# Kernel optimization log

Hardware: AMD Instinct MI355X
Metric: run time of the kernel (lower is better)

The kernel has to match this reference:

```python
import jax, jax.numpy as jnp
import numpy as np

N_HEAD = 16
N_EMBD = 1024
B, T = 4, 1024


def setup_inputs() -> dict:
    key = jax.random.key(0)
    ks = jax.random.split(key, 8)
    hs = N_EMBD // N_HEAD
    x = jax.random.normal(ks[0], (B, T, N_EMBD), dtype=jnp.float32)
    # previous-layer attention load per token, ~O(1/T) like a softmax column mean
    refractory_state = jax.random.uniform(ks[1], (B, T), dtype=jnp.float32) / T
    s_attn = 1.0 / np.sqrt(N_EMBD)
    W_attn = jax.random.normal(ks[2], (N_EMBD, 3 * N_EMBD), dtype=jnp.float32) * s_attn
    b_attn = jnp.zeros((3 * N_EMBD,), dtype=jnp.float32)
    W_proj = jax.random.normal(ks[3], (N_EMBD, N_EMBD), dtype=jnp.float32) * s_attn
    b_proj = jnp.zeros((N_EMBD,), dtype=jnp.float32)
    # learnable LIF params, init per module (lif_mode='refractory')
    threshold = jnp.full((N_HEAD,), 0.01, dtype=jnp.float32)
    leak = jnp.full((N_HEAD,), 2.0, dtype=jnp.float32)
    steepness = jnp.full((N_HEAD,), 2.0, dtype=jnp.float32)
    ref_strength = jnp.full((N_HEAD,), -2.0, dtype=jnp.float32)
    cross_w = jnp.full((N_HEAD,), -2.0, dtype=jnp.float32)
    return {
        "x": x, "refractory_state": refractory_state,
        "W_attn": W_attn, "b_attn": b_attn,
        "W_proj": W_proj, "b_proj": b_proj,
        "threshold": threshold, "leak": leak, "steepness": steepness,
        "ref_strength": ref_strength, "cross_w": cross_w,
    }


def reference(x, refractory_state, W_attn, b_attn, W_proj, b_proj,
              threshold, leak, steepness, ref_strength, cross_w):
    Bq, Tq, C = x.shape
    H = N_HEAD
    hs = C // H
    qkv = x @ W_attn + b_attn                     # [B,T,3C]
    q, k, v = jnp.split(qkv, 3, axis=-1)
    q = q.reshape(Bq, Tq, H, hs).transpose(0, 2, 1, 3)  # [B,H,T,hs]
    k = k.reshape(Bq, Tq, H, hs).transpose(0, 2, 1, 3)
    v = v.reshape(Bq, Tq, H, hs).transpose(0, 2, 1, 3)

    att = jnp.einsum('bhqd,bhkd->bhqk', q, k) * (1.0 / jnp.sqrt(jnp.asarray(hs, x.dtype)))
    causal = jnp.tril(jnp.ones((Tq, Tq), dtype=bool))
    att = jnp.where(causal[None, None], att, -jnp.inf)
    probs = jax.nn.softmax(att, axis=-1)          # [B,H,T,T]

    thr = (jnp.abs(threshold) * 0.1)[None, :, None, None]
    lk = jax.nn.sigmoid(leak)[None, :, None, None]
    st = jax.nn.softplus(steepness)[None, :, None, None]
    # refractory: column load over queries + cross-layer load
    column_load = probs.mean(axis=-2, keepdims=True)          # [B,H,1,T]
    eff_thr = thr + jax.nn.softplus(ref_strength)[None, :, None, None] * column_load
    eff_thr = eff_thr + jax.nn.sigmoid(cross_w)[None, :, None, None] * refractory_state[:, None, None, :]

    fire = jax.nn.sigmoid(st * (probs - eff_thr))
    lif_w = fire + lk * (1.0 - fire)
    mod = probs * lif_w
    mod = mod / (mod.sum(axis=-1, keepdims=True) + 1e-8)
    new_refractory = mod.mean(axis=1).mean(axis=-2)           # [B,T]

    y = jnp.einsum('bhqk,bhkd->bhqd', mod, v)
    y = y.transpose(0, 2, 1, 3).reshape(Bq, Tq, C)
    y = y @ W_proj + b_proj
    return y, new_refractory
```

## Files before the change

kernel.cpp:

```cpp
#include <hip/hip_runtime.h>
#include <math.h>

#define B_  4
#define T_  1024
#define C_  1024
#define H_  16
#define HS_ 64
#define K2E 0.1803368801f
#define LOG2E 1.44269504f

typedef _Float16 f16;
typedef _Float16 f16x8 __attribute__((ext_vector_type(8)));
typedef float f32x4 __attribute__((ext_vector_type(4)));

#define MFMA16(a,b,c) __builtin_amdgcn_mfma_f32_16x16x32_f16(a,b,c,0,0,0)
#define EXP2(x) __builtin_amdgcn_exp2f(x)
#define RCP(x)  __builtin_amdgcn_rcpf(x)

__device__ __forceinline__ void gload16(const f16* g, f16* l){
    __builtin_amdgcn_global_load_lds(
        (const __attribute__((address_space(1))) void*)g,
        (__attribute__((address_space(3))) void*)l, 16, 0, 0);
}

__device__ __forceinline__ float qsum_(float v){
    v += __shfl_xor(v,1,64); v += __shfl_xor(v,2,64);
    v += __shfl_xor(v,4,64); v += __shfl_xor(v,8,64);
    return v;
}
__device__ __forceinline__ float sigmoidf_(float x){ return 1.0f/(1.0f + __expf(-x)); }
__device__ __forceinline__ float softplusf_(float x){ return fmaxf(x, 0.0f) + log1pf(__expf(-fabsf(x))); }

__global__ __launch_bounds__(256) void conv_f16_k(
    const float* __restrict__ in, f16* __restrict__ out, int n8)
{
    int i = blockIdx.x*256 + threadIdx.x;
    if (i < n8){
        const float4* p = (const float4*)in + (size_t)i*2;
        float4 a = p[0], b = p[1];
        f16x8 o;
        o[0]=(f16)a.x; o[1]=(f16)a.y; o[2]=(f16)a.z; o[3]=(f16)a.w;
        o[4]=(f16)b.x; o[5]=(f16)b.y; o[6]=(f16)b.z; o[7]=(f16)b.w;
        *((f16x8*)out + i) = o;
    }
}

__global__ __launch_bounds__(256) void transpose_f16_k(
    const float* __restrict__ in, f16* __restrict__ out, int K, int N)
{
    __shared__ float tl[32][33];
    const int n0 = blockIdx.x*32, k0 = blockIdx.y*32;
    const int c = threadIdx.x & 31, r4 = threadIdx.x >> 5;
    #pragma unroll
    for (int i=0;i<4;i++){
        int r = r4*4 + i;
        tl[r][c] = in[(size_t)(k0+r)*N + n0 + c];
    }
    __syncthreads();
    #pragma unroll
    for (int i=0;i<4;i++){
        int r = r4*4 + i;
        out[(size_t)(n0+r)*K + k0 + c] = (f16)tl[c][r];
    }
}

__global__ __launch_bounds__(256) void gemm_qkv_k(
    const f16* __restrict__ A, const f16* __restrict__ Bt,
    const float* __restrict__ bias,
    f16* __restrict__ Qh, f16* __restrict__ Kh, f16* __restrict__ Vt)
{
    __shared__ __align__(16) f16 Al[8*512];
    __shared__ __align__(16) f16 Bl[8*512];
    const int tid = threadIdx.x;
    const int lane = tid & 63, wave = tid >> 6;
    const int lx = lane & 15, quad = lane >> 4;
    const int wm = wave & 1, wn = wave >> 1;
    const int m0 = blockIdx.y*128, n0 = blockIdx.x*128;
    f32x4 acc[4][4];
    #pragma unroll
    for (int i=0;i<4;i++){
        #pragma unroll
        for (int j=0;j<4;j++){ acc[i][j][0]=0.f;acc[i][j][1]=0.f;acc[i][j][2]=0.f;acc[i][j][3]=0.f; }
    }
    for (int k0=0; k0<1024; k0+=32){
        __syncthreads();
        #pragma unroll
        for (int i=0;i<2;i++){
            int c = i*4 + wave;
            gload16(A  + (size_t)(m0 + c*16 + lx)*1024 + k0 + quad*8, &Al[c*512]);
            gload16(Bt + (size_t)(n0 + c*16 + lx)*1024 + k0 + quad*8, &Bl[c*512]);
        }
        __syncthreads();
        f16x8 af[4], bf[4];
        #pragma unroll
        for (int mt=0;mt<4;mt++) af[mt] = *(const f16x8*)&Al[(wm*4+mt)*512 + quad*128 + lx*8];
        #pragma unroll
        for (int nt=0;nt<4;nt++) bf[nt] = *(const f16x8*)&Bl[(wn*4+nt)*512 + quad*128 + lx*8];
        #pragma unroll
        for (int mt=0;mt<4;mt++){
            #pragma unroll
            for (int nt=0;nt<4;nt++)
                acc[mt][nt] = MFMA16(af[mt], bf[nt], acc[mt][nt]);
        }
    }
    #pragma unroll
    for (int mt=0;mt<4;mt++){
        #pragma unroll
        for (int nt=0;nt<4;nt++){
            int n = n0 + wn*64 + nt*16 + lx;
            int which = n >> 10, cc = n & 1023, h = cc >> 6, d = cc & 63;
            float bv = bias[n];
            #pragma unroll
            for (int r=0;r<4;r++){
                int m = m0 + wm*64 + mt*16 + quad*4 + r;
                int bb = m >> 10, t = m & 1023;
                int bh = bb*16 + h;
                float v = acc[mt][nt][r] + bv;
                if (which==0)      Qh[((size_t)bh*1024 + t)*64 + d] = (f16)v;
                else if (which==1) Kh[((size_t)bh*1024 + t)*64 + d] = (f16)v;
                else               Vt[((size_t)bh*64 + d)*1024 + t] = (f16)v;
            }
        }
    }
}

__global__ __launch_bounds__(256) void gemm_proj_k(
    const f16* __restrict__ A, const f16* __restrict__ Bt,
    const float* __restrict__ bias, float* __restrict__ out)
{
    __shared__ __align__(16) f16 Al[8*512];
    __shared__ __align__(16) f16 Bl[4*512];
    const int tid = threadIdx.x;
    const int lane = tid & 63, wave = tid >> 6;
    const int lx = lane & 15, quad = lane >> 4;
    const int wm = wave & 1, wn = wave >> 1;
    const int m0 = blockIdx.y*128, n0 = blockIdx.x*64;
    f32x4 acc[4][2];
    #pragma unroll
    for (int i=0;i<4;i++){
        #pragma unroll
        for (int j=0;j<2;j++){ acc[i][j][0]=0.f;acc[i][j][1]=0.f;acc[i][j][2]=0.f;acc[i][j][3]=0.f; }
    }
    for (int k0=0; k0<1024; k0+=32){
        __syncthreads();
        #pragma unroll
        for (int i=0;i<3;i++){
            int u = i*4 + wave;
            if (u < 8)
                gload16(A  + (size_t)(m0 + u*16 + lx)*1024 + k0 + quad*8, &Al[u*512]);
            else
                gload16(Bt + (size_t)(n0 + (u-8)*16 + lx)*1024 + k0 + quad*8, &Bl[(u-8)*512]);
        }
        __syncthreads();
        f16x8 af[4], bf[2];
        #pragma unroll
        for (int mt=0;mt<4;mt++) af[mt] = *(const f16x8*)&Al[(wm*4+mt)*512 + quad*128 + lx*8];
        #pragma unroll
        for (int nt=0;nt<2;nt++) bf[nt] = *(const f16x8*)&Bl[(wn*2+nt)*512 + quad*128 + lx*8];
        #pragma unroll
        for (int mt=0;mt<4;mt++){
            #pragma unroll
            for (int nt=0;nt<2;nt++)
                acc[mt][nt] = MFMA16(af[mt], bf[nt], acc[mt][nt]);
        }
    }
    #pragma unroll
    for (int mt=0;mt<4;mt++){
        #pragma unroll
        for (int nt=0;nt<2;nt++){
            int n = n0 + wn*32 + nt*16 + lx;
            float bv = bias[n];
            #pragma unroll
            for (int r=0;r<4;r++){
                int m = m0 + wm*64 + mt*16 + quad*4 + r;
                out[(size_t)m*1024 + n] = acc[mt][nt][r] + bv;
            }
        }
    }
}

__global__ __launch_bounds__(256) void attn_stats_k(
    const f16* __restrict__ Qh, const f16* __restrict__ Kh,
    float* __restrict__ rowl, float* __restrict__ colp)
{
    __shared__ __align__(16) f16 Kl[4096];
    __shared__ float colacc[64];
    const int tid = threadIdx.x;
    const int lane = tid & 63, wave = tid >> 6;
    const int lx = lane & 15, quad = lane >> 4;
    const int g  = 15 - (blockIdx.x >> 6);
    const int bh = blockIdx.x & 63;
    const int qpos = wave*16 + quad*4;

    const size_t qoff = ((size_t)bh*1024 + g*64 + wave*16 + lx)*64;
    f16x8 aq0 = *(const f16x8*)(Qh + qoff + quad*8);
    f16x8 aq1 = *(const f16x8*)(Qh + qoff + 32 + quad*8);

    float ls[4] = {0.f,0.f,0.f,0.f};
    for (int kt=0; kt<=g; kt++){
        __syncthreads();
        #pragma unroll
        for (int i=0;i<2;i++){
            int u = i*4 + wave, c = u & 3, kh = u >> 2;
            gload16(Kh + ((size_t)bh*1024 + kt*64 + c*16 + lx)*64 + kh*32 + quad*8,
                    &Kl[c*1024 + kh*512]);
        }
        __syncthreads();
        const bool diag = (kt == g);
        #pragma unroll
        for (int nt=0;nt<4;nt++){
            f32x4 sc = {0.f,0.f,0.f,0.f};
            f16x8 b0 = *(const f16x8*)&Kl[nt*1024 + quad*128 + lx*8];
            f16x8 b1 = *(const f16x8*)&Kl[nt*1024 + (4+quad)*128 + lx*8];
            sc = MFMA16(aq0, b0, sc);
            sc = MFMA16(aq1, b1, sc);
            #pragma unroll
            for (int r=0;r<4;r++){
                float sv = sc[r];
                if (diag && (nt*16+lx) > (qpos + r)) sv = -1e4f;
                ls[r] += EXP2(sv*K2E);
            }
        }
    }
    float invl[4];
    #pragma unroll
    for (int r=0;r<4;r++){
        float l = qsum_(ls[r]);
        if (lx == 0) rowl[(size_t)bh*1024 + g*64 + qpos + r] = l;
        invl[r] = RCP(l);
    }

    for (int kt=0; kt<=g; kt++){
        __syncthreads();
        #pragma unroll
        for (int i=0;i<2;i++){
            int u = i*4 + wave, c = u & 3, kh = u >> 2;
            gload16(Kh + ((size_t)bh*1024 + kt*64 + c*16 + lx)*64 + kh*32 + quad*8,
                    &Kl[c*1024 + kh*512]);
        }
        if (tid < 64) colacc[tid] = 0.f;
        __syncthreads();
        const bool diag = (kt == g);
        #pragma unroll
        for (int nt=0;nt<4;nt++){
            f32x4 sc = {0.f,0.f,0.f,0.f};
            f16x8 b0 = *(const f16x8*)&Kl[nt*1024 + quad*128 + lx*8];
            f16x8 b1 = *(const f16x8*)&Kl[nt*1024 + (4+quad)*128 + lx*8];
            sc = MFMA16(aq0, b0, sc);
            sc = MFMA16(aq1, b1, sc);
            float csum = 0.f;
            #pragma unroll
            for (int r=0;r<4;r++){
                float sv = sc[r];
                if (diag && (nt*16+lx) > (qpos + r)) sv = -1e4f;
                csum += EXP2(sv*K2E) * invl[r];
            }
            csum += __shfl_xor(csum,16,64); csum += __shfl_xor(csum,32,64);
            if (quad == 0) atomicAdd(&colacc[nt*16+lx], csum);
        }
        __syncthreads();
        if (tid < 64) atomicAdd(&colp[(size_t)bh*1024 + kt*64 + tid], colacc[tid]);
    }
}

__global__ __launch_bounds__(256) void attn_apply_k(
    const f16* __restrict__ Qh, const f16* __restrict__ Kh, const f16* __restrict__ Vt,
    const float* __restrict__ rowl,
    const float* __restrict__ colp, const float* __restrict__ refr,
    const float* __restrict__ threshold, const float* __restrict__ leak,
    const float* __restrict__ steepness, const float* __restrict__ ref_strength,
    const float* __restrict__ cross_w,
    f16* __restrict__ Yh, float* __restrict__ racc)
{
    __shared__ __align__(16) f16 Kl[4096];
    __shared__ __align__(16) f16 Vl[4096];
    __shared__ __align__(16) f16 Pl[4][16*72];
    __shared__ float eb[1024];
    __shared__ float colacc[64];
    const int tid = threadIdx.x;
    const int lane = tid & 63, wave = tid >> 6;
    const int lx = lane & 15, quad = lane >> 4;
    const int g  = 15 - (blockIdx.x >> 6);
    const int bh = blockIdx.x & 63;
    const int b  = bh >> 4, h = bh & 15;
    const int qpos = wave*16 + quad*4;

    const float thr = fabsf(threshold[h])*0.1f;
    const float lk  = sigmoidf_(leak[h]);
    const float st2 = softplusf_(steepness[h]) * LOG2E;
    const float sprT= softplusf_(ref_strength[h]) * (1.0f/T_);
    const float cw  = sigmoidf_(cross_w[h]);
    const float Alk = 1.f - lk;

    {
        float4 cp = *(const float4*)(colp + (size_t)bh*1024 + tid*4);
        float4 rf = *(const float4*)(refr + (size_t)b*1024 + tid*4);
        eb[tid*4+0] = thr + sprT*cp.x + cw*rf.x;
        eb[tid*4+1] = thr + sprT*cp.y + cw*rf.y;
        eb[tid*4+2] = thr + sprT*cp.z + cw*rf.z;
        eb[tid*4+3] = thr + sprT*cp.w + cw*rf.w;
    }

    const size_t qoff = ((size_t)bh*1024 + g*64 + wave*16 + lx)*64;
    f16x8 aq0 = *(const f16x8*)(Qh + qoff + quad*8);
    f16x8 aq1 = *(const f16x8*)(Qh + qoff + 32 + quad*8);

    float invl[4];
    #pragma unroll
    for (int r=0;r<4;r++)
        invl[r] = RCP(rowl[(size_t)bh*1024 + g*64 + qpos + r]);

    f32x4 y[4];
    #pragma unroll
    for (int i=0;i<4;i++){ y[i][0]=0.f;y[i][1]=0.f;y[i][2]=0.f;y[i][3]=0.f; }
    float Dp[4] = {0.f,0.f,0.f,0.f};

    for (int kt=0; kt<=g; kt++){
        __syncthreads();
        #pragma unroll
        for (int i=0;i<4;i++){
            int u = i*4 + wave;
            if (u < 8){
                int c = u & 3, kh = u >> 2;
                gload16(Kh + ((size_t)bh*1024 + kt*64 + c*16 + lx)*64 + kh*32 + quad*8,
                        &Kl[c*1024 + kh*512]);
            } else {
                int v = u - 8, c = v & 3, kh = v >> 2;
                gload16(Vt + ((size_t)bh*64 + c*16 + lx)*1024 + kt*64 + kh*32 + quad*8,
                        &Vl[c*1024 + kh*512]);
            }
        }
        __syncthreads();
        const bool diag = (kt == g);
        #pragma unroll
        for (int nt=0;nt<4;nt++){
            f32x4 sc = {0.f,0.f,0.f,0.f};
            f16x8 b0 = *(const f16x8*)&Kl[nt*1024 + quad*128 + lx*8];
            f16x8 b1 = *(const f16x8*)&Kl[nt*1024 + (4+quad)*128 + lx*8];
            sc = MFMA16(aq0, b0, sc);
            sc = MFMA16(aq1, b1, sc);
            float ec = st2 * eb[kt*64 + nt*16 + lx];
            #pragma unroll
            for (int r=0;r<4;r++){
                float sv = sc[r];
                if (diag && (nt*16+lx) > (qpos + r)) sv = -1e4f;
                float p = EXP2(sv*K2E) * invl[r];
                float e2 = EXP2(ec - st2*p);
                float fire = RCP(1.f + e2);
                float pw = p * (lk + Alk*fire);
                Dp[r] += pw;
                Pl[wave][(quad*4+r)*72 + nt*16 + lx] = (f16)pw;
            }
        }
        f16x8 ap0 = *(const f16x8*)&Pl[wave][lx*72 + quad*8];
        f16x8 ap1 = *(const f16x8*)&Pl[wave][lx*72 + 32 + quad*8];
        #pragma unroll
        for (int dt=0;dt<4;dt++){
            f16x8 bv0 = *(const f16x8*)&Vl[dt*1024 + quad*128 + lx*8];
            f16x8 bv1 = *(const f16x8*)&Vl[dt*1024 + (4+quad)*128 + lx*8];
            y[dt] = MFMA16(ap0, bv0, y[dt]);
            y[dt] = MFMA16(ap1, bv1, y[dt]);
        }
    }
    float invD[4];
    #pragma unroll
    for (int r=0;r<4;r++) invD[r] = RCP(qsum_(Dp[r]) + 1e-8f);
    #pragma unroll
    for (int dt=0;dt<4;dt++){
        #pragma unroll
        for (int r=0;r<4;r++){
            Yh[(size_t)(b*1024 + g*64 + wave*16 + quad*4 + r)*1024 + h*64 + dt*16 + lx]
                = (f16)(y[dt][r]*invD[r]);
        }
    }

    for (int kt=0; kt<=g; kt++){
        __syncthreads();
        #pragma unroll
        for (int i=0;i<2;i++){
            int u = i*4 + wave, c = u & 3, kh = u >> 2;
            gload16(Kh + ((size_t)bh*1024 + kt*64 + c*16 + lx)*64 + kh*32 + quad*8,
                    &Kl[c*1024 + kh*512]);
        }
        if (tid < 64) colacc[tid] = 0.f;
        __syncthreads();
        const bool diag = (kt == g);
        #pragma unroll
        for (int nt=0;nt<4;nt++){
            f32x4 sc = {0.f,0.f,0.f,0.f};
            f16x8 b0 = *(const f16x8*)&Kl[nt*1024 + quad*128 + lx*8];
            f16x8 b1 = *(const f16x8*)&Kl[nt*1024 + (4+quad)*128 + lx*8];
            sc = MFMA16(aq0, b0, sc);
            sc = MFMA16(aq1, b1, sc);
            float ec = st2 * eb[kt*64 + nt*16 + lx];
            float csum = 0.f;
            #pragma unroll
            for (int r=0;r<4;r++){
                float sv = sc[r];
                if (diag && (nt*16+lx) > (qpos + r)) sv = -1e4f;
                float p = EXP2(sv*K2E) * invl[r];
                float e2 = EXP2(ec - st2*p);
                float fire = RCP(1.f + e2);
                csum += p * (lk + Alk*fire) * invD[r];
            }
            csum += __shfl_xor(csum,16,64); csum += __shfl_xor(csum,32,64);
            if (quad == 0) atomicAdd(&colacc[nt*16+lx], csum);
        }
        __syncthreads();
        if (tid < 64) atomicAdd(&racc[(size_t)b*1024 + kt*64 + tid], colacc[tid]);
    }
}

__global__ __launch_bounds__(256) void finish_refr_k(
    const float* __restrict__ racc, float* __restrict__ out)
{
    int i = blockIdx.x*256 + threadIdx.x;
    if (i < B_*T_) out[i] = racc[i] * (1.0f/(H_*T_));
}

extern "C" void kernel_launch(void* const* d_in, const int* in_sizes, int n_in,
                              void* d_out, int out_size, void* d_ws, size_t ws_size,
                              hipStream_t stream) {
    (void)in_sizes; (void)n_in; (void)out_size; (void)ws_size;
    const float* x           = (const float*)d_in[0];
    const float* refr        = (const float*)d_in[1];
    const float* W_attn      = (const float*)d_in[2];
    const float* b_attn      = (const float*)d_in[3];
    const float* W_proj      = (const float*)d_in[4];
    const float* b_proj      = (const float*)d_in[5];
    const float* threshold   = (const float*)d_in[6];
    const float* leak        = (const float*)d_in[7];
    const float* steepness   = (const float*)d_in[8];
    const float* ref_strength= (const float*)d_in[9];
    const float* cross_w     = (const float*)d_in[10];
    float* out = (float*)d_out;

    char* ws = (char*)d_ws;
    f16* x_h = (f16*)ws;                       ws += (size_t)4096*1024*2;
    f16* WaT = (f16*)ws;                       ws += (size_t)3072*1024*2;
    f16* WpT = (f16*)ws;                       ws += (size_t)1024*1024*2;
    f16* Qh  = (f16*)ws;                       ws += (size_t)64*1024*64*2;
    f16* Kh  = (f16*)ws;                       ws += (size_t)64*1024*64*2;
    f16* Vt  = (f16*)ws;                       ws += (size_t)64*64*1024*2;
    f16* Yh  = (f16*)ws;                       ws += (size_t)4096*1024*2;
    float* rowl = (float*)ws;                  ws += (size_t)65536*4;
    float* colp = (float*)ws;                  ws += (size_t)65536*4;
    float* racc = (float*)ws;                  ws += (size_t)4096*4;

    hipMemsetAsync(colp, 0, 65536*sizeof(float), stream);
    hipMemsetAsync(racc, 0, 4096*sizeof(float), stream);

    conv_f16_k<<<dim3(2048), dim3(256), 0, stream>>>(x, x_h, 4096*1024/8);
    transpose_f16_k<<<dim3(96,32), dim3(256), 0, stream>>>(W_attn, WaT, 1024, 3072);
    transpose_f16_k<<<dim3(32,32), dim3(256), 0, stream>>>(W_proj, WpT, 1024, 1024);
    gemm_qkv_k<<<dim3(24,32), dim3(256), 0, stream>>>(x_h, WaT, b_attn, Qh, Kh, Vt);
    attn_stats_k<<<dim3(1024), dim3(256), 0, stream>>>(Qh, Kh, rowl, colp);
    attn_apply_k<<<dim3(1024), dim3(256), 0, stream>>>(
        Qh, Kh, Vt, rowl, colp, refr,
        threshold, leak, steepness, ref_strength, cross_w, Yh, racc);
    gemm_proj_k<<<dim3(16,32), dim3(256), 0, stream>>>(Yh, WpT, b_proj, out);
    finish_refr_k<<<dim3(16), dim3(256), 0, stream>>>(racc, out + (size_t)B_*T_*C_);
}
```

Baseline: 319.1 us.

## Register-prefetch GEMM tiles, drop LDS staging in attention, precompute effective thresholds

The QKV and projection GEMMs now load the next K-tile into registers while the current tile is computed, replacing direct global-to-LDS loads. The QKV GEMM also uses a wider K step and a grouped block-index swizzle for L2 reuse. The attention kernels read K and V fragments straight from global memory instead of staging them through shared memory, which removes the per-tile barriers. Column sums now go into a per-block 1024-entry LDS accumulator that is flushed once at the end. A new small kernel precomputes the scaled effective threshold per (b,h,k), so the apply kernel no longer rebuilds it, at the cost of an extra launch and more global or cache traffic for the K, V and threshold reads.

```diff
diff --git a/kernel.cpp b/kernel.cpp
--- a/kernel.cpp
+++ b/kernel.cpp
@@ -16,12 +16,6 @@
 #define MFMA16(a,b,c) __builtin_amdgcn_mfma_f32_16x16x32_f16(a,b,c,0,0,0)
 #define EXP2(x) __builtin_amdgcn_exp2f(x)
 #define RCP(x)  __builtin_amdgcn_rcpf(x)
-
-__device__ __forceinline__ void gload16(const f16* g, f16* l){
-    __builtin_amdgcn_global_load_lds(
-        (const __attribute__((address_space(1))) void*)g,
-        (__attribute__((address_space(3))) void*)l, 16, 0, 0);
-}
 
 __device__ __forceinline__ float qsum_(float v){
     v += __shfl_xor(v,1,64); v += __shfl_xor(v,2,64);
@@ -69,38 +63,59 @@
     const float* __restrict__ bias,
     f16* __restrict__ Qh, f16* __restrict__ Kh, f16* __restrict__ Vt)
 {
-    __shared__ __align__(16) f16 Al[8*512];
-    __shared__ __align__(16) f16 Bl[8*512];
+    __shared__ __align__(16) f16 Al[8192];
+    __shared__ __align__(16) f16 Bl[8192];
     const int tid = threadIdx.x;
     const int lane = tid & 63, wave = tid >> 6;
     const int lx = lane & 15, quad = lane >> 4;
     const int wm = wave & 1, wn = wave >> 1;
-    const int m0 = blockIdx.y*128, n0 = blockIdx.x*128;
+    const int bid = blockIdx.x;
+    const int grp = bid >> 5, w = bid & 31;
+    const int m0 = ((grp/6)*8 + (w>>2))*128;
+    const int n0 = ((grp%6)*4 + (w&3))*128;
     f32x4 acc[4][4];
     #pragma unroll
     for (int i=0;i<4;i++){
         #pragma unroll
         for (int j=0;j<4;j++){ acc[i][j][0]=0.f;acc[i][j][1]=0.f;acc[i][j][2]=0.f;acc[i][j][3]=0.f; }
     }
-    for (int k0=0; k0<1024; k0+=32){
+    f16x8 ra[4], rb[4];
+    #pragma unroll
+    for (int i=0;i<4;i++){
+        int u = i*4 + wave, rg = u>>1, kh = u&1;
+        ra[i] = *(const f16x8*)(A  + (size_t)(m0+rg*16+lx)*1024 + kh*32 + quad*8);
+        rb[i] = *(const f16x8*)(Bt + (size_t)(n0+rg*16+lx)*1024 + kh*32 + quad*8);
+    }
+    for (int k0=0; k0<1024; k0+=64){
         __syncthreads();
         #pragma unroll
-        for (int i=0;i<2;i++){
-            int c = i*4 + wave;
-            gload16(A  + (size_t)(m0 + c*16 + lx)*1024 + k0 + quad*8, &Al[c*512]);
-            gload16(Bt + (size_t)(n0 + c*16 + lx)*1024 + k0 + quad*8, &Bl[c*512]);
+        for (int i=0;i<4;i++){
+            int u = i*4 + wave, rg = u>>1, kh = u&1;
+            *(f16x8*)&Al[rg*1024 + kh*512 + quad*128 + lx*8] = ra[i];
+            *(f16x8*)&Bl[rg*1024 + kh*512 + quad*128 + lx*8] = rb[i];
         }
         __syncthreads();
-        f16x8 af[4], bf[4];
-        #pragma unroll
-        for (int mt=0;mt<4;mt++) af[mt] = *(const f16x8*)&Al[(wm*4+mt)*512 + quad*128 + lx*8];
-        #pragma unroll
-        for (int nt=0;nt<4;nt++) bf[nt] = *(const f16x8*)&Bl[(wn*4+nt)*512 + quad*128 + lx*8];
-        #pragma unroll
-        for (int mt=0;mt<4;mt++){
-            #pragma unroll
-            for (int nt=0;nt<4;nt++)
-                acc[mt][nt] = MFMA16(af[mt], bf[nt], acc[mt][nt]);
+        if (k0 + 64 < 1024){
+            #pragma unroll
+            for (int i=0;i<4;i++){
+                int u = i*4 + wave, rg = u>>1, kh = u&1;
+                ra[i] = *(const f16x8*)(A  + (size_t)(m0+rg*16+lx)*1024 + k0+64 + kh*32 + quad*8);
+                rb[i] = *(const f16x8*)(Bt + (size_t)(n0+rg*16+lx)*1024 + k0+64 + kh*32 + quad*8);
+            }
+        }
+        #pragma unroll
+        for (int ks=0;ks<2;ks++){
+            f16x8 af[4], bf[4];
+            #pragma unroll
+            for (int mt=0;mt<4;mt++) af[mt] = *(const f16x8*)&Al[(wm*4+mt)*1024 + ks*512 + quad*128 + lx*8];
+            #pragma unroll
+            for (int nt=0;nt<4;nt++) bf[nt] = *(const f16x8*)&Bl[(wn*4+nt)*1024 + ks*512 + quad*128 + lx*8];
+            #pragma unroll
+            for (int mt=0;mt<4;mt++){
+                #pragma unroll
+                for (int nt=0;nt<4;nt++)
+                    acc[mt][nt] = MFMA16(af[mt], bf[nt], acc[mt][nt]);
+            }
         }
     }
     #pragma unroll
@@ -141,17 +156,24 @@
         #pragma unroll
         for (int j=0;j<2;j++){ acc[i][j][0]=0.f;acc[i][j][1]=0.f;acc[i][j][2]=0.f;acc[i][j][3]=0.f; }
     }
+    f16x8 ra[2], rb;
+    #pragma unroll
+    for (int i=0;i<2;i++)
+        ra[i] = *(const f16x8*)(A + (size_t)(m0 + (i*4+wave)*16 + lx)*1024 + quad*8);
+    rb = *(const f16x8*)(Bt + (size_t)(n0 + wave*16 + lx)*1024 + quad*8);
     for (int k0=0; k0<1024; k0+=32){
         __syncthreads();
         #pragma unroll
-        for (int i=0;i<3;i++){
-            int u = i*4 + wave;
-            if (u < 8)
-                gload16(A  + (size_t)(m0 + u*16 + lx)*1024 + k0 + quad*8, &Al[u*512]);
-            else
-                gload16(Bt + (size_t)(n0 + (u-8)*16 + lx)*1024 + k0 + quad*8, &Bl[(u-8)*512]);
-        }
+        for (int i=0;i<2;i++)
+            *(f16x8*)&Al[(i*4+wave)*512 + quad*128 + lx*8] = ra[i];
+        *(f16x8*)&Bl[wave*512 + quad*128 + lx*8] = rb;
         __syncthreads();
+        if (k0 + 32 < 1024){
+            #pragma unroll
+            for (int i=0;i<2;i++)
+                ra[i] = *(const f16x8*)(A + (size_t)(m0 + (i*4+wave)*16 + lx)*1024 + k0+32 + quad*8);
+            rb = *(const f16x8*)(Bt + (size_t)(n0 + wave*16 + lx)*1024 + k0+32 + quad*8);
+        }
         f16x8 af[4], bf[2];
         #pragma unroll
         for (int mt=0;mt<4;mt++) af[mt] = *(const f16x8*)&Al[(wm*4+mt)*512 + quad*128 + lx*8];
@@ -183,14 +205,16 @@
     const f16* __restrict__ Qh, const f16* __restrict__ Kh,
     float* __restrict__ rowl, float* __restrict__ colp)
 {
-    __shared__ __align__(16) f16 Kl[4096];
-    __shared__ float colacc[64];
+    __shared__ float cacc[1024];
     const int tid = threadIdx.x;
     const int lane = tid & 63, wave = tid >> 6;
     const int lx = lane & 15, quad = lane >> 4;
     const int g  = 15 - (blockIdx.x >> 6);
     const int bh = blockIdx.x & 63;
     const int qpos = wave*16 + quad*4;
+    const size_t kbase = (size_t)bh*65536;
+
+    for (int i=tid; i<(g+1)*64; i+=256) cacc[i] = 0.f;
 
     const size_t qoff = ((size_t)bh*1024 + g*64 + wave*16 + lx)*64;
     f16x8 aq0 = *(const f16x8*)(Qh + qoff + quad*8);
@@ -198,20 +222,13 @@
 
     float ls[4] = {0.f,0.f,0.f,0.f};
     for (int kt=0; kt<=g; kt++){
-        __syncthreads();
-        #pragma unroll
-        for (int i=0;i<2;i++){
-            int u = i*4 + wave, c = u & 3, kh = u >> 2;
-            gload16(Kh + ((size_t)bh*1024 + kt*64 + c*16 + lx)*64 + kh*32 + quad*8,
-                    &Kl[c*1024 + kh*512]);
-        }
-        __syncthreads();
         const bool diag = (kt == g);
         #pragma unroll
         for (int nt=0;nt<4;nt++){
+            const f16* kp = Kh + kbase + (size_t)(kt*64 + nt*16 + lx)*64 + quad*8;
+            f16x8 b0 = *(const f16x8*)kp;
+            f16x8 b1 = *(const f16x8*)(kp + 32);
             f32x4 sc = {0.f,0.f,0.f,0.f};
-            f16x8 b0 = *(const f16x8*)&Kl[nt*1024 + quad*128 + lx*8];
-            f16x8 b1 = *(const f16x8*)&Kl[nt*1024 + (4+quad)*128 + lx*8];
             sc = MFMA16(aq0, b0, sc);
             sc = MFMA16(aq1, b1, sc);
             #pragma unroll
@@ -229,23 +246,16 @@
         if (lx == 0) rowl[(size_t)bh*1024 + g*64 + qpos + r] = l;
         invl[r] = RCP(l);
     }
+    __syncthreads();
 
     for (int kt=0; kt<=g; kt++){
-        __syncthreads();
-        #pragma unroll
-        for (int i=0;i<2;i++){
-            int u = i*4 + wave, c = u & 3, kh = u >> 2;
-            gload16(Kh + ((size_t)bh*1024 + kt*64 + c*16 + lx)*64 + kh*32 + quad*8,
-                    &Kl[c*1024 + kh*512]);
-        }
-        if (tid < 64) colacc[tid] = 0.f;
-        __syncthreads();
         const bool diag = (kt == g);
         #pragma unroll
         for (int nt=0;nt<4;nt++){
+            const f16* kp = Kh + kbase + (size_t)(kt*64 + nt*16 + lx)*64 + quad*8;
+            f16x8 b0 = *(const f16x8*)kp;
+            f16x8 b1 = *(const f16x8*)(kp + 32);
             f32x4 sc = {0.f,0.f,0.f,0.f};
-            f16x8 b0 = *(const f16x8*)&Kl[nt*1024 + quad*128 + lx*8];
-            f16x8 b1 = *(const f16x8*)&Kl[nt*1024 + (4+quad)*128 + lx*8];
             sc = MFMA16(aq0, b0, sc);
             sc = MFMA16(aq1, b1, sc);
             float csum = 0.f;
@@ -256,27 +266,37 @@
                 csum += EXP2(sv*K2E) * invl[r];
             }
             csum += __shfl_xor(csum,16,64); csum += __shfl_xor(csum,32,64);
-            if (quad == 0) atomicAdd(&colacc[nt*16+lx], csum);
-        }
-        __syncthreads();
-        if (tid < 64) atomicAdd(&colp[(size_t)bh*1024 + kt*64 + tid], colacc[tid]);
-    }
+            if (quad == 0) atomicAdd(&cacc[kt*64 + nt*16 + lx], csum);
+        }
+    }
+    __syncthreads();
+    for (int i=tid; i<(g+1)*64; i+=256) atomicAdd(&colp[(size_t)bh*1024 + i], cacc[i]);
+}
+
+__global__ __launch_bounds__(256) void prep_eb_k(
+    const float* __restrict__ colp, const float* __restrict__ refr,
+    const float* __restrict__ threshold, const float* __restrict__ steepness,
+    const float* __restrict__ ref_strength, const float* __restrict__ cross_w,
+    float* __restrict__ ebs)
+{
+    int idx = blockIdx.x*256 + threadIdx.x;
+    int bh = idx >> 10, k = idx & 1023;
+    int b = bh >> 4, h = bh & 15;
+    float thr = fabsf(threshold[h])*0.1f;
+    float st2 = softplusf_(steepness[h]) * LOG2E;
+    float sprT = softplusf_(ref_strength[h]) * (1.0f/T_);
+    float cw = sigmoidf_(cross_w[h]);
+    ebs[idx] = st2*(thr + sprT*colp[idx] + cw*refr[b*1024 + k]);
 }
 
 __global__ __launch_bounds__(256) void attn_apply_k(
     const f16* __restrict__ Qh, const f16* __restrict__ Kh, const f16* __restrict__ Vt,
-    const float* __restrict__ rowl,
-    const float* __restrict__ colp, const float* __restrict__ refr,
-    const float* __restrict__ threshold, const float* __restrict__ leak,
-    const float* __restrict__ steepness, const float* __restrict__ ref_strength,
-    const float* __restrict__ cross_w,
+    const float* __restrict__ rowl, const float* __restrict__ ebs,
+    const float* __restrict__ leak, const float* __restrict__ steepness,
     f16* __restrict__ Yh, float* __restrict__ racc)
 {
-    __shared__ __align__(16) f16 Kl[4096];
-    __shared__ __align__(16) f16 Vl[4096];
     __shared__ __align__(16) f16 Pl[4][16*72];
-    __shared__ float eb[1024];
-    __shared__ float colacc[64];
+    __shared__ float cacc[1024];
     const int tid = threadIdx.x;
     const int lane = tid & 63, wave = tid >> 6;
     const int lx = lane & 15, quad = lane >> 4;
@@ -284,22 +304,14 @@
     const int bh = blockIdx.x & 63;
     const int b  = bh >> 4, h = bh & 15;
     const int qpos = wave*16 + quad*4;
-
-    const float thr = fabsf(threshold[h])*0.1f;
+    const size_t kbase = (size_t)bh*65536;
+
     const float lk  = sigmoidf_(leak[h]);
     const float st2 = softplusf_(steepness[h]) * LOG2E;
-    const float sprT= softplusf_(ref_strength[h]) * (1.0f/T_);
-    const float cw  = sigmoidf_(cross_w[h]);
     const float Alk = 1.f - lk;
 
-    {
-        float4 cp = *(const float4*)(colp + (size_t)bh*1024 + tid*4);
-        float4 rf = *(const float4*)(refr + (size_t)b*1024 + tid*4);
-        eb[tid*4+0] = thr + sprT*cp.x + cw*rf.x;
-        eb[tid*4+1] = thr + sprT*cp.y + cw*rf.y;
-        eb[tid*4+2] = thr + sprT*cp.z + cw*rf.z;
-        eb[tid*4+3] = thr + sprT*cp.w + cw*rf.w;
-    }
+    for (int i=tid; i<(g+1)*64; i+=256) cacc[i] = 0.f;
+    __syncthreads();
 
     const size_t qoff = ((size_t)bh*1024 + g*64 + wave*16 + lx)*64;
     f16x8 aq0 = *(const f16x8*)(Qh + qoff + quad*8);
@@ -316,37 +328,22 @@
     float Dp[4] = {0.f,0.f,0.f,0.f};
 
     for (int kt=0; kt<=g; kt++){
-        __syncthreads();
-        #pragma unroll
-        for (int i=0;i<4;i++){
-            int u = i*4 + wave;
-            if (u < 8){
-                int c = u & 3, kh = u >> 2;
-                gload16(Kh + ((size_t)bh*1024 + kt*64 + c*16 + lx)*64 + kh*32 + quad*8,
-                        &Kl[c*1024 + kh*512]);
-            } else {
-                int v = u - 8, c = v & 3, kh = v >> 2;
-                gload16(Vt + ((size_t)bh*64 + c*16 + lx)*1024 + kt*64 + kh*32 + quad*8,
-                        &Vl[c*1024 + kh*512]);
-            }
-        }
-        __syncthreads();
         const bool diag = (kt == g);
         #pragma unroll
         for (int nt=0;nt<4;nt++){
+            const f16* kp = Kh + kbase + (size_t)(kt*64 + nt*16 + lx)*64 + quad*8;
+            f16x8 b0 = *(const f16x8*)kp;
+            f16x8 b1 = *(const f16x8*)(kp + 32);
             f32x4 sc = {0.f,0.f,0.f,0.f};
-            f16x8 b0 = *(const f16x8*)&Kl[nt*1024 + quad*128 + lx*8];
-            f16x8 b1 = *(const f16x8*)&Kl[nt*1024 + (4+quad)*128 + lx*8];
             sc = MFMA16(aq0, b0, sc);
             sc = MFMA16(aq1, b1, sc);
-            float ec = st2 * eb[kt*64 + nt*16 + lx];
+            float ec = ebs[(size_t)bh*1024 + kt*64 + nt*16 + lx];
             #pragma unroll
             for (int r=0;r<4;r++){
                 float sv = sc[r];
                 if (diag && (nt*16+lx) > (qpos + r)) sv = -1e4f;
                 float p = EXP2(sv*K2E) * invl[r];
-                float e2 = EXP2(ec - st2*p);
-                float fire = RCP(1.f + e2);
+                float fire = RCP(1.f + EXP2(ec - st2*p));
                 float pw = p * (lk + Alk*fire);
                 Dp[r] += pw;
                 Pl[wave][(quad*4+r)*72 + nt*16 + lx] = (f16)pw;
@@ -356,8 +353,9 @@
         f16x8 ap1 = *(const f16x8*)&Pl[wave][lx*72 + 32 + quad*8];
         #pragma unroll
         for (int dt=0;dt<4;dt++){
-            f16x8 bv0 = *(const f16x8*)&Vl[dt*1024 + quad*128 + lx*8];
-            f16x8 bv1 = *(const f16x8*)&Vl[dt*1024 + (4+quad)*128 + lx*8];
+            const f16* vp = Vt + (size_t)(bh*64 + dt*16 + lx)*1024 + kt*64 + quad*8;
+            f16x8 bv0 = *(const f16x8*)vp;
+            f16x8 bv1 = *(const f16x8*)(vp + 32);
             y[dt] = MFMA16(ap0, bv0, y[dt]);
             y[dt] = MFMA16(ap1, bv1, y[dt]);
         }
@@ -375,40 +373,31 @@
     }
 
     for (int kt=0; kt<=g; kt++){
-        __syncthreads();
-        #pragma unroll
-        for (int i=0;i<2;i++){
-            int u = i*4 + wave, c = u & 3, kh = u >> 2;
-            gload16(Kh + ((size_t)bh*1024 + kt*64 + c*16 + lx)*64 + kh*32 + quad*8,
-                    &Kl[c*1024 + kh*512]);
-        }
-        if (tid < 64) colacc[tid] = 0.f;
-        __syncthreads();
         const bool diag = (kt == g);
         #pragma unroll
         for (int nt=0;nt<4;nt++){
+            const f16* kp = Kh + kbase + (size_t)(kt*64 + nt*16 + lx)*64 + quad*8;
+            f16x8 b0 = *(const f16x8*)kp;
+            f16x8 b1 = *(const f16x8*)(kp + 32);
             f32x4 sc = {0.f,0.f,0.f,0.f};
-            f16x8 b0 = *(const f16x8*)&Kl[nt*1024 + quad*128 + lx*8];
-            f16x8 b1 = *(const f16x8*)&Kl[nt*1024 + (4+quad)*128 + lx*8];
             sc = MFMA16(aq0, b0, sc);
             sc = MFMA16(aq1, b1, sc);
-            float ec = st2 * eb[kt*64 + nt*16 + lx];
+            float ec = ebs[(size_t)bh*1024 + kt*64 + nt*16 + lx];
             float csum = 0.f;
             #pragma unroll
             for (int r=0;r<4;r++){
                 float sv = sc[r];
                 if (diag && (nt*16+lx) > (qpos + r)) sv = -1e4f;
                 float p = EXP2(sv*K2E) * invl[r];
-                float e2 = EXP2(ec - st2*p);
-                float fire = RCP(1.f + e2);
+                float fire = RCP(1.f + EXP2(ec - st2*p));
                 csum += p * (lk + Alk*fire) * invD[r];
             }
             csum += __shfl_xor(csum,16,64); csum += __shfl_xor(csum,32,64);
-            if (quad == 0) atomicAdd(&colacc[nt*16+lx], csum);
-        }
-        __syncthreads();
-        if (tid < 64) atomicAdd(&racc[(size_t)b*1024 + kt*64 + tid], colacc[tid]);
-    }
+            if (quad == 0) atomicAdd(&cacc[kt*64 + nt*16 + lx], csum);
+        }
+    }
+    __syncthreads();
+    for (int i=tid; i<(g+1)*64; i+=256) atomicAdd(&racc[(size_t)b*1024 + i], cacc[i]);
 }
 
 __global__ __launch_bounds__(256) void finish_refr_k(
@@ -445,6 +434,7 @@
     f16* Yh  = (f16*)ws;                       ws += (size_t)4096*1024*2;
     float* rowl = (float*)ws;                  ws += (size_t)65536*4;
     float* colp = (float*)ws;                  ws += (size_t)65536*4;
+    float* ebs  = (float*)ws;                  ws += (size_t)65536*4;
     float* racc = (float*)ws;                  ws += (size_t)4096*4;
 
     hipMemsetAsync(colp, 0, 65536*sizeof(float), stream);
@@ -453,11 +443,12 @@
     conv_f16_k<<<dim3(2048), dim3(256), 0, stream>>>(x, x_h, 4096*1024/8);
     transpose_f16_k<<<dim3(96,32), dim3(256), 0, stream>>>(W_attn, WaT, 1024, 3072);
     transpose_f16_k<<<dim3(32,32), dim3(256), 0, stream>>>(W_proj, WpT, 1024, 1024);
-    gemm_qkv_k<<<dim3(24,32), dim3(256), 0, stream>>>(x_h, WaT, b_attn, Qh, Kh, Vt);
+    gemm_qkv_k<<<dim3(768), dim3(256), 0, stream>>>(x_h, WaT, b_attn, Qh, Kh, Vt);
     attn_stats_k<<<dim3(1024), dim3(256), 0, stream>>>(Qh, Kh, rowl, colp);
+    prep_eb_k<<<dim3(256), dim3(256), 0, stream>>>(colp, refr, threshold, steepness,
+                                                   ref_strength, cross_w, ebs);
     attn_apply_k<<<dim3(1024), dim3(256), 0, stream>>>(
-        Qh, Kh, Vt, rowl, colp, refr,
-        threshold, leak, steepness, ref_strength, cross_w, Yh, racc);
+        Qh, Kh, Vt, rowl, ebs, leak, steepness, Yh, racc);
     gemm_proj_k<<<dim3(16,32), dim3(256), 0, stream>>>(Yh, WpT, b_proj, out);
     finish_refr_k<<<dim3(16), dim3(256), 0, stream>>>(racc, out + (size_t)B_*T_*C_);
 }
```

After: 398.0 us. 1.25x slower.
